# Kernel optimization log

Measured on AMD Instinct MI355X. Metric: run time of the kernel, lower is better.

Reference implementation:

```python
import jax, jax.numpy as jnp
import numpy as np

HEADS = 8

def _rotate_every_two(t):
    # t: [..., d]; interleaved rotation (-x2, x1) pairs
    x1 = t[..., ::2]
    x2 = t[..., 1::2]
    return jnp.stack([-x2, x1], axis=-1).reshape(t.shape)

def _theta_shift(t, sin, cos):
    return t * cos + _rotate_every_two(t) * sin

def setup_inputs() -> dict:
    key = jax.random.key(0)
    ks = jax.random.split(key, 5)
    B, H, W, C = 4, 40, 40, 512
    dh = C // HEADS
    x = jax.random.normal(ks[0], (B, H, W, C), dtype=jnp.float32)
    sin = jax.random.normal(ks[1], (H, W, dh), dtype=jnp.float32)
    cos = jax.random.normal(ks[2], (H, W, dh), dtype=jnp.float32)
    # 1x1 conv weight [3C, C] (kernel dims squeezed) + bias
    w_qkv = jax.random.normal(ks[3], (3 * C, C), dtype=jnp.float32) * (C ** -0.5)
    b_qkv = jnp.zeros((3 * C,), dtype=jnp.float32)
    return {"x": x, "sin": sin, "cos": cos, "w_qkv": w_qkv, "b_qkv": b_qkv}

def reference(x, sin, cos, w_qkv, b_qkv):
    B, H, W, C = x.shape
    heads = HEADS
    dh = C // heads
    scale = dh ** -0.5
    # 1x1 conv == per-pixel linear projection
    qkv = jnp.einsum('bhwc,oc->bhwo', x, w_qkv) + b_qkv  # [B,H,W,3C]
    q, k, v = jnp.split(qkv, 3, axis=-1)

    def to_heads(t):
        # channel order is (heads, dim_head) per the torch rearrange
        return t.reshape(B, H, W, heads, dh).transpose(0, 3, 1, 2, 4)  # [B,heads,H,W,dh]

    q = _theta_shift(to_heads(q), sin, cos)
    k = _theta_shift(to_heads(k), sin, cos)
    # v is computed but unused downstream in the original module (bug preserved)

    N = H * W
    q = q.reshape(B, heads, N, dh)
    k = k.reshape(B, heads, N, dh)

    attn = jnp.einsum('bhnd,bhmd->bhnm', q, k) * scale  # [B,heads,N,N]
    p = jax.nn.softmax(attn, axis=-1)
    # NOTE: original code does matmul(logist, kfine_heads) — K, not V. Kept faithful.
    out = jnp.einsum('bhnm,bhmd->bhnd', p, k)  # [B,heads,N,dh]
    out = out.transpose(0, 2, 1, 3).reshape(B, H, W, C)
    return out
```

## Files before the change

kernel.cpp:

```cpp
#include <hip/hip_runtime.h>
#include <hip/hip_bf16.h>


typedef __hip_bfloat16 bf16;
typedef __attribute__((ext_vector_type(8))) short short8;
typedef __attribute__((ext_vector_type(4))) short bfx4;
typedef __attribute__((ext_vector_type(4))) float f32x4;

#define NSP 1600
#define CDIM 512
#define DH 64

__device__ __forceinline__ f32x4 mfma32(short8 a, short8 b, f32x4 c) {
  return __builtin_amdgcn_mfma_f32_16x16x32_bf16(a, b, c, 0, 0, 0);
}

#if __has_builtin(__builtin_amdgcn_mfma_f32_16x16x16bf16_1k)
__device__ __forceinline__ f32x4 mfma_k16(bfx4 a, bfx4 b, f32x4 c) {
  return __builtin_amdgcn_mfma_f32_16x16x16bf16_1k(a, b, c, 0, 0, 0);
}
#else
__device__ __forceinline__ f32x4 mfma_k16(bfx4 a, bfx4 b, f32x4 c) {
  short8 a8 = {a.x, a.y, a.z, a.w, 0, 0, 0, 0};
  short8 b8 = {b.x, b.y, b.z, b.w, 0, 0, 0, 0};
  return __builtin_amdgcn_mfma_f32_16x16x32_bf16(a8, b8, c, 0, 0, 0);
}
#endif

__device__ __forceinline__ short8 cvt8(float4 v0, float4 v1) {
  short8 r; bf16* p = (bf16*)&r;
  p[0] = __float2bfloat16(v0.x); p[1] = __float2bfloat16(v0.y);
  p[2] = __float2bfloat16(v0.z); p[3] = __float2bfloat16(v0.w);
  p[4] = __float2bfloat16(v1.x); p[5] = __float2bfloat16(v1.y);
  p[6] = __float2bfloat16(v1.z); p[7] = __float2bfloat16(v1.w);
  return r;
}

extern "C" __global__ __launch_bounds__(256)
void cvt_kernel(const float* __restrict__ x, const float* __restrict__ w,
                const float* __restrict__ sin_t, const float* __restrict__ cos_t,
                bf16* __restrict__ x_bf, bf16* __restrict__ w_bf,
                float* __restrict__ sinT, float* __restrict__ cosT)
{
  __shared__ float t_lds[64][68];
  const int bid = blockIdx.x, tid = threadIdx.x;
  if (bid < 1600) {
    const size_t i = (size_t)bid * 2048 + tid * 8;
    float4 v0 = *(const float4*)(x + i);
    float4 v1 = *(const float4*)(x + i + 4);
    *(short8*)(x_bf + i) = cvt8(v0, v1);
  } else if (bid < 1856) {
    const size_t i = (size_t)(bid - 1600) * 2048 + tid * 8;
    float4 v0 = *(const float4*)(w + i);
    float4 v1 = *(const float4*)(w + i + 4);
    *(short8*)(w_bf + i) = cvt8(v0, v1);
  } else {
    const int t = bid - 1856;
    const float* src = (t < 25) ? sin_t : cos_t;
    float* dst = (t < 25) ? sinT : cosT;
    const int nt = (t < 25) ? t : t - 25;
    const int r = tid >> 2, c = (tid & 3) * 16;
#pragma unroll
    for (int j = 0; j < 4; ++j)
      *(float4*)&t_lds[r][c + j * 4] =
          *(const float4*)(src + (size_t)(nt * 64 + r) * 64 + c + j * 4);
    __syncthreads();
#pragma unroll
    for (int j4 = 0; j4 < 4; ++j4) {
      float4 o;
      o.x = t_lds[c + j4 * 4 + 0][r];
      o.y = t_lds[c + j4 * 4 + 1][r];
      o.z = t_lds[c + j4 * 4 + 2][r];
      o.w = t_lds[c + j4 * 4 + 3][r];
      *(float4*)(dst + (size_t)r * NSP + nt * 64 + c + j4 * 4) = o;
    }
  }
}

extern "C" __global__ __launch_bounds__(256)
void proj_kernel(const bf16* __restrict__ x_bf, const bf16* __restrict__ w_bf,
                 const float* __restrict__ bias, const float* __restrict__ sinT,
                 const float* __restrict__ cosT, bf16* __restrict__ q_ws,
                 bf16* __restrict__ k2_ws, bf16* __restrict__ kt2_ws)
{
  __shared__ __align__(16) char smem[36864];
  bf16 (*x_lds)[72] = (bf16(*)[72])smem;
  bf16 (*w_lds)[72] = (bf16(*)[72])(smem + 18432);
  bf16* ep = (bf16*)smem;

  const int tid  = threadIdx.x;
  const int wave = tid >> 6;
  const int lane = tid & 63;
  const int col  = lane & 15;
  const int quad = lane >> 4;
  const int wm = wave >> 1, wo = wave & 1;
  const int m0 = blockIdx.x * 128;
  const int o0 = blockIdx.y * 128;

  f32x4 acc[4][4];
#pragma unroll
  for (int i = 0; i < 4; ++i)
#pragma unroll
    for (int j = 0; j < 4; ++j) acc[i][j] = {0.f, 0.f, 0.f, 0.f};

  const int srow = tid >> 1;
  const int sch  = (tid & 1) * 32;

  for (int kt = 0; kt < 8; ++kt) {
    __syncthreads();
    {
      const bf16* xs = x_bf + (size_t)(m0 + srow) * CDIM + kt * 64 + sch;
      const bf16* ws = w_bf + (size_t)(o0 + srow) * CDIM + kt * 64 + sch;
#pragma unroll
      for (int j = 0; j < 4; ++j) {
        *(short8*)&x_lds[srow][sch + j * 8] = *(const short8*)(xs + j * 8);
        *(short8*)&w_lds[srow][sch + j * 8] = *(const short8*)(ws + j * 8);
      }
    }
    __syncthreads();
#pragma unroll
    for (int half = 0; half < 2; ++half) {
      short8 af[4], bfr[4];
#pragma unroll
      for (int mt = 0; mt < 4; ++mt)
        af[mt] = *(short8*)&x_lds[wm * 64 + mt * 16 + col][half * 32 + quad * 8];
#pragma unroll
      for (int ot = 0; ot < 4; ++ot)
        bfr[ot] = *(short8*)&w_lds[wo * 64 + ot * 16 + col][half * 32 + quad * 8];
#pragma unroll
      for (int mt = 0; mt < 4; ++mt)
#pragma unroll
        for (int ot = 0; ot < 4; ++ot)
          acc[mt][ot] = mfma32(af[mt], bfr[ot], acc[mt][ot]);
    }
  }

  __syncthreads();
  const int b_idx = (m0 + wm * 64) / NSP;
  const int n0w   = m0 + wm * 64 - b_idx * NSP;
  const bool isq  = (o0 < 512);
#pragma unroll
  for (int ot = 0; ot < 4; ++ot) {
    const int o_local = wo * 64 + ot * 16 + col;
    const int o_g = o0 + o_local;
    const float bv = bias[o_g];
    const int d = o_g & 63;
#pragma unroll
    for (int mt = 0; mt < 4; ++mt) {
      const int nl = mt * 16 + quad * 4;
      float t[4], rot[4];
#pragma unroll
      for (int r = 0; r < 4; ++r) t[r] = acc[mt][ot][r] + bv;
#pragma unroll
      for (int r = 0; r < 4; ++r) {
        float tp = __shfl_xor(t[r], 1, 64);
        rot[r] = (lane & 1) ? tp : -tp;
      }
      const float4 c4 = *(const float4*)(cosT + (size_t)d * NSP + n0w + nl);
      const float4 s4 = *(const float4*)(sinT + (size_t)d * NSP + n0w + nl);
      float res[4];
      res[0] = t[0] * c4.x + rot[0] * s4.x;
      res[1] = t[1] * c4.y + rot[1] * s4.y;
      res[2] = t[2] * c4.z + rot[2] * s4.z;
      res[3] = t[3] * c4.w + rot[3] * s4.w;
      if (isq) {
#pragma unroll
        for (int r = 0; r < 4; ++r) res[r] *= 0.125f;
      }
      bfx4 pk; bf16* pp = (bf16*)&pk;
#pragma unroll
      for (int r = 0; r < 4; ++r) pp[r] = __float2bfloat16(res[r]);
      *(bfx4*)&ep[o_local * 132 + wm * 64 + nl] = pk;
    }
  }
  __syncthreads();

  if (isq) {
    const int m_l = tid >> 1, half = tid & 1;
    const int gm = m0 + m_l;
    const int bi = gm / NSP, n = gm - bi * NSP;
    const int h = (o0 >> 6) + half;
    bf16* base = q_ws + ((size_t)(bi * 8 + h) * NSP + n) * 64;
#pragma unroll
    for (int c = 0; c < 8; ++c) {
      short8 v; bf16* vp = (bf16*)&v;
#pragma unroll
      for (int j = 0; j < 8; ++j) vp[j] = ep[(half * 64 + c * 8 + j) * 132 + m_l];
      *(short8*)(base + c * 8) = v;
    }
  } else {
    const int h0 = (o0 - 512) >> 6;
#pragma unroll
    for (int it = 0; it < 8; ++it) {
      const int ci = it * 256 + tid;
      const int hh = ci >> 10, T = (ci >> 9) & 1, inner = ci & 511;
      const int ccol = inner & 15, cq = (inner >> 4) & 3;
      const int f = (inner >> 6) & 1, ti = (inner >> 7) & 1, kh2 = (inner >> 8) & 1;
      const int gmb = m0 + T * 64;
      const int bi = gmb / NSP, ktile = (gmb - bi * NSP) >> 6;
      const int m_l = T * 64 + (2 * kh2 + ti) * 16 + ccol;
      const int er0 = hh * 64 + (f * 4 + cq) * 8;
      short8 v; bf16* vp = (bf16*)&v;
#pragma unroll
      for (int j = 0; j < 8; ++j) vp[j] = ep[(er0 + j) * 132 + m_l];
      *(short8*)(k2_ws +
          (((size_t)(bi * 8 + h0 + hh) * 25 + ktile) * 512 + inner) * 8) = v;
    }
#pragma unroll
    for (int it = 0; it < 8; ++it) {
      const int ci = it * 256 + tid;
      const int hh = ci >> 10, T = (ci >> 9) & 1, inner = ci & 511;
      const int ccol = inner & 15, cq = (inner >> 4) & 3;
      const int dt = (inner >> 6) & 3, kh2 = (inner >> 8) & 1;
      const int gmb = m0 + T * 64;
      const int bi = gmb / NSP, ktile = (gmb - bi * NSP) >> 6;
      const bf16* eprow =
          ep + (hh * 64 + dt * 16 + ccol) * 132 + T * 64 + kh2 * 32 + cq * 4;
      short8 v;
      ((bfx4*)&v)[0] = *(const bfx4*)(eprow);
      ((bfx4*)&v)[1] = *(const bfx4*)(eprow + 16);
      *(short8*)(kt2_ws +
          (((size_t)(bi * 8 + h0 + hh) * 25 + ktile) * 512 + inner) * 8) = v;
    }
  }
}

extern "C" __global__ __launch_bounds__(256)
void attn_kernel(const bf16* __restrict__ q_ws, const bf16* __restrict__ k2_ws,
                 const bf16* __restrict__ kt2_ws, float* __restrict__ out)
{
  __shared__ float red[2][64][36];

  const int qt = blockIdx.x, bh = blockIdx.y;
  const int b = bh >> 3, h = bh & 7;
  const int tid  = threadIdx.x;
  const int wave = tid >> 6;
  const int lane = tid & 63;
  const int col  = lane & 15;
  const int quad = lane >> 4;
  const int qg = wave & 1, kh = wave >> 1;

  short8 qb[2][2];
#pragma unroll
  for (int ct = 0; ct < 2; ++ct) {
    const bf16* qp =
        q_ws + ((size_t)bh * NSP + qt * 64 + (qg * 2 + ct) * 16 + col) * 64;
    qb[ct][0] = *(const short8*)(qp + quad * 8);
    qb[ct][1] = *(const short8*)(qp + 32 + quad * 8);
  }

  f32x4 oacc[4][2];
#pragma unroll
  for (int i = 0; i < 4; ++i)
#pragma unroll
    for (int j = 0; j < 2; ++j) oacc[i][j] = {0.f, 0.f, 0.f, 0.f};
  float l_part[2] = {0.f, 0.f};

  const bf16* k2b  = k2_ws  + (size_t)bh * 25 * 4096;
  const bf16* kt2b = kt2_ws + (size_t)bh * 25 * 4096;

  for (int kt = 0; kt < 25; ++kt) {
    const bf16* kc  = k2b  + kt * 4096;
    const bf16* kc2 = kt2b + kt * 4096;

    short8 kf[2][2];
#pragma unroll
    for (int ti = 0; ti < 2; ++ti)
#pragma unroll
      for (int f = 0; f < 2; ++f)
        kf[ti][f] =
            *(const short8*)(kc + (((kh * 2 + ti) * 2 + f) * 64 + lane) * 8);
    short8 ktf[4];
#pragma unroll
    for (int dt = 0; dt < 4; ++dt)
      ktf[dt] = *(const short8*)(kc2 + ((kh * 4 + dt) * 64 + lane) * 8);

    f32x4 s[2][2];
#pragma unroll
    for (int ti = 0; ti < 2; ++ti)
#pragma unroll
      for (int ct = 0; ct < 2; ++ct) {
        f32x4 t = {0.f, 0.f, 0.f, 0.f};
        t = mfma32(kf[ti][0], qb[ct][0], t);
        t = mfma32(kf[ti][1], qb[ct][1], t);
        s[ti][ct] = t;
      }

    bfx4 p4[2][2];
#pragma unroll
    for (int ti = 0; ti < 2; ++ti)
#pragma unroll
      for (int ct = 0; ct < 2; ++ct) {
#pragma unroll
        for (int r = 0; r < 4; ++r) s[ti][ct][r] = __expf(s[ti][ct][r]);
        l_part[ct] += s[ti][ct][0] + s[ti][ct][1] + s[ti][ct][2] + s[ti][ct][3];
        bf16* pp = (bf16*)&p4[ti][ct];
#pragma unroll
        for (int r = 0; r < 4; ++r) pp[r] = __float2bfloat16(s[ti][ct][r]);
      }

#pragma unroll
    for (int dt = 0; dt < 4; ++dt) {
      bfx4 alo = __builtin_shufflevector(ktf[dt], ktf[dt], 0, 1, 2, 3);
      bfx4 ahi = __builtin_shufflevector(ktf[dt], ktf[dt], 4, 5, 6, 7);
#pragma unroll
      for (int ct = 0; ct < 2; ++ct) {
        oacc[dt][ct] = mfma_k16(alo, p4[0][ct], oacc[dt][ct]);
        oacc[dt][ct] = mfma_k16(ahi, p4[1][ct], oacc[dt][ct]);
      }
    }
  }

#pragma unroll
  for (int ct = 0; ct < 2; ++ct) {
    l_part[ct] += __shfl_xor(l_part[ct], 16, 64);
    l_part[ct] += __shfl_xor(l_part[ct], 32, 64);
  }

  if (wave >= 2) {
    float* dst = &red[wave - 2][lane][0];
#pragma unroll
    for (int dt = 0; dt < 4; ++dt)
#pragma unroll
      for (int ct = 0; ct < 2; ++ct)
        *(f32x4*)(dst + (dt * 2 + ct) * 4) = oacc[dt][ct];
    dst[32] = l_part[0]; dst[33] = l_part[1];
  }
  __syncthreads();
  if (wave < 2) {
    const float* srcr = &red[wave][lane][0];
#pragma unroll
    for (int dt = 0; dt < 4; ++dt)
#pragma unroll
      for (int ct = 0; ct < 2; ++ct)
        oacc[dt][ct] += *(const f32x4*)(srcr + (dt * 2 + ct) * 4);
    const float inv0 = 1.f / (l_part[0] + srcr[32]);
    const float inv1 = 1.f / (l_part[1] + srcr[33]);
#pragma unroll
    for (int ct = 0; ct < 2; ++ct) {
      const float inv = ct ? inv1 : inv0;
      const int qrow = qt * 64 + (qg * 2 + ct) * 16 + col;
      float* ob = out + ((size_t)b * NSP + qrow) * CDIM + h * 64;
#pragma unroll
      for (int dt = 0; dt < 4; ++dt) {
        float4 v;
        v.x = oacc[dt][ct][0] * inv; v.y = oacc[dt][ct][1] * inv;
        v.z = oacc[dt][ct][2] * inv; v.w = oacc[dt][ct][3] * inv;
        *(float4*)(ob + dt * 16 + quad * 4) = v;
      }
    }
  }
}

extern "C" void kernel_launch(void* const* d_in, const int* in_sizes, int n_in,
                              void* d_out, int out_size, void* d_ws, size_t ws_size,
                              hipStream_t stream) {
  const float* x     = (const float*)d_in[0];
  const float* sin_t = (const float*)d_in[1];
  const float* cos_t = (const float*)d_in[2];
  const float* w_qkv = (const float*)d_in[3];
  const float* b_qkv = (const float*)d_in[4];
  float* out = (float*)d_out;

  const size_t QK = (size_t)32 * NSP * DH;
  bf16* q_ws   = (bf16*)d_ws;
  bf16* k2_ws  = q_ws + QK;
  bf16* kt2_ws = k2_ws + QK;
  bf16* x_bf   = kt2_ws + QK;
  bf16* w_bf   = x_bf + (size_t)6400 * CDIM;
  float* sinT  = (float*)(w_bf + (size_t)1024 * CDIM);
  float* cosT  = sinT + (size_t)DH * NSP;

  cvt_kernel<<<1906, 256, 0, stream>>>(x, w_qkv, sin_t, cos_t, x_bf, w_bf, sinT, cosT);

  dim3 gproj(50, 8);
  proj_kernel<<<gproj, 256, 0, stream>>>(x_bf, w_bf, b_qkv, sinT, cosT,
                                         q_ws, k2_ws, kt2_ws);

  dim3 gattn(25, 32);
  attn_kernel<<<gattn, 256, 0, stream>>>(q_ws, k2_ws, kt2_ws, out);
}
```

Before: 139.5 us.

## Split attention key tiles across eight waves with two-stage cross-wave reduction

The attention kernel now launches 512 threads (8 waves) per block instead of 4. Each wave handles one 16-key sub-tile instead of two, so the per-wave MFMA chain per key tile is halved. Partial outputs and row sums are combined in LDS through a two-stage tree reduction. The aim is more waves in flight to hide latency on a grid of only 800 blocks, at the cost of an extra barrier, more LDS, and redundant Q loads per wave.

```diff
diff --git a/kernel.cpp b/kernel.cpp
--- a/kernel.cpp
+++ b/kernel.cpp
@@ -225,11 +225,11 @@
   }
 }
 
-extern "C" __global__ __launch_bounds__(256)
+extern "C" __global__ __launch_bounds__(512, 6)
 void attn_kernel(const bf16* __restrict__ q_ws, const bf16* __restrict__ k2_ws,
                  const bf16* __restrict__ kt2_ws, float* __restrict__ out)
 {
-  __shared__ float red[2][64][36];
+  __shared__ float red[4][64][36];
 
   const int qt = blockIdx.x, bh = blockIdx.y;
   const int b = bh >> 3, h = bh & 7;
@@ -238,7 +238,8 @@
   const int lane = tid & 63;
   const int col  = lane & 15;
   const int quad = lane >> 4;
-  const int qg = wave & 1, kh = wave >> 1;
+  const int qg = wave & 1;
+  const int kh = wave >> 1;
 
   short8 qb[2][2];
 #pragma unroll
@@ -258,57 +259,46 @@
 
   const bf16* k2b  = k2_ws  + (size_t)bh * 25 * 4096;
   const bf16* kt2b = kt2_ws + (size_t)bh * 25 * 4096;
+  const int khh = kh >> 1, khl = kh & 1;
 
   for (int kt = 0; kt < 25; ++kt) {
     const bf16* kc  = k2b  + kt * 4096;
     const bf16* kc2 = kt2b + kt * 4096;
 
-    short8 kf[2][2];
-#pragma unroll
-    for (int ti = 0; ti < 2; ++ti)
-#pragma unroll
-      for (int f = 0; f < 2; ++f)
-        kf[ti][f] =
-            *(const short8*)(kc + (((kh * 2 + ti) * 2 + f) * 64 + lane) * 8);
-    short8 ktf[4];
-#pragma unroll
-    for (int dt = 0; dt < 4; ++dt)
-      ktf[dt] = *(const short8*)(kc2 + ((kh * 4 + dt) * 64 + lane) * 8);
-
-    f32x4 s[2][2];
-#pragma unroll
-    for (int ti = 0; ti < 2; ++ti)
-#pragma unroll
-      for (int ct = 0; ct < 2; ++ct) {
-        f32x4 t = {0.f, 0.f, 0.f, 0.f};
-        t = mfma32(kf[ti][0], qb[ct][0], t);
-        t = mfma32(kf[ti][1], qb[ct][1], t);
-        s[ti][ct] = t;
-      }
-
-    bfx4 p4[2][2];
-#pragma unroll
-    for (int ti = 0; ti < 2; ++ti)
-#pragma unroll
-      for (int ct = 0; ct < 2; ++ct) {
-#pragma unroll
-        for (int r = 0; r < 4; ++r) s[ti][ct][r] = __expf(s[ti][ct][r]);
-        l_part[ct] += s[ti][ct][0] + s[ti][ct][1] + s[ti][ct][2] + s[ti][ct][3];
-        bf16* pp = (bf16*)&p4[ti][ct];
-#pragma unroll
-        for (int r = 0; r < 4; ++r) pp[r] = __float2bfloat16(s[ti][ct][r]);
-      }
-
-#pragma unroll
-    for (int dt = 0; dt < 4; ++dt) {
-      bfx4 alo = __builtin_shufflevector(ktf[dt], ktf[dt], 0, 1, 2, 3);
-      bfx4 ahi = __builtin_shufflevector(ktf[dt], ktf[dt], 4, 5, 6, 7);
-#pragma unroll
-      for (int ct = 0; ct < 2; ++ct) {
-        oacc[dt][ct] = mfma_k16(alo, p4[0][ct], oacc[dt][ct]);
-        oacc[dt][ct] = mfma_k16(ahi, p4[1][ct], oacc[dt][ct]);
-      }
-    }
+    short8 kf[2];
+#pragma unroll
+    for (int f = 0; f < 2; ++f)
+      kf[f] = *(const short8*)(kc + (((kh * 2 + f) * 64) + lane) * 8);
+    bfx4 ktf[4];
+#pragma unroll
+    for (int dt = 0; dt < 4; ++dt)
+      ktf[dt] = *(const bfx4*)(kc2 + (((khh * 4 + dt) * 64 + lane) * 8) + khl * 4);
+
+    f32x4 s[2];
+#pragma unroll
+    for (int ct = 0; ct < 2; ++ct) {
+      f32x4 t = {0.f, 0.f, 0.f, 0.f};
+      t = mfma32(kf[0], qb[ct][0], t);
+      t = mfma32(kf[1], qb[ct][1], t);
+      s[ct] = t;
+    }
+
+    bfx4 p4[2];
+#pragma unroll
+    for (int ct = 0; ct < 2; ++ct) {
+#pragma unroll
+      for (int r = 0; r < 4; ++r) s[ct][r] = __expf(s[ct][r]);
+      l_part[ct] += s[ct][0] + s[ct][1] + s[ct][2] + s[ct][3];
+      bf16* pp = (bf16*)&p4[ct];
+#pragma unroll
+      for (int r = 0; r < 4; ++r) pp[r] = __float2bfloat16(s[ct][r]);
+    }
+
+#pragma unroll
+    for (int dt = 0; dt < 4; ++dt)
+#pragma unroll
+      for (int ct = 0; ct < 2; ++ct)
+        oacc[dt][ct] = mfma_k16(ktf[dt], p4[ct], oacc[dt][ct]);
   }
 
 #pragma unroll
@@ -317,7 +307,27 @@
     l_part[ct] += __shfl_xor(l_part[ct], 32, 64);
   }
 
-  if (wave >= 2) {
+  if (wave >= 4) {
+    float* dst = &red[wave - 4][lane][0];
+#pragma unroll
+    for (int dt = 0; dt < 4; ++dt)
+#pragma unroll
+      for (int ct = 0; ct < 2; ++ct)
+        *(f32x4*)(dst + (dt * 2 + ct) * 4) = oacc[dt][ct];
+    dst[32] = l_part[0]; dst[33] = l_part[1];
+  }
+  __syncthreads();
+  if (wave < 4) {
+    const float* srcr = &red[wave][lane][0];
+#pragma unroll
+    for (int dt = 0; dt < 4; ++dt)
+#pragma unroll
+      for (int ct = 0; ct < 2; ++ct)
+        oacc[dt][ct] += *(const f32x4*)(srcr + (dt * 2 + ct) * 4);
+    l_part[0] += srcr[32]; l_part[1] += srcr[33];
+  }
+  __syncthreads();
+  if (wave == 2 || wave == 3) {
     float* dst = &red[wave - 2][lane][0];
 #pragma unroll
     for (int dt = 0; dt < 4; ++dt)
@@ -378,5 +388,5 @@
                                          q_ws, k2_ws, kt2_ws);
 
   dim3 gattn(25, 32);
-  attn_kernel<<<gattn, 256, 0, stream>>>(q_ws, k2_ws, kt2_ws, out);
-}
+  attn_kernel<<<gattn, 512, 0, stream>>>(q_ws, k2_ws, kt2_ws, out);
+}
```

New measurement: 149.6 us. 1.07x slower.

## Double-buffer K fragment loads and remap attention grid for XCD locality

Applied to the files above, without the earlier changes.

The attention loop now prefetches the next key tile's register fragments while computing on the current one, using two register buffers in a manually unrolled ping-pong loop. This is meant to hide global load latency behind the MFMA and exp work. The grid becomes a 1D launch of 800 blocks, with block index mapped so that consecutive IDs modulo 8 land on different batch-heads. This likely aims to keep all blocks of a given batch-head on the same XCD so they share its L2. The cost is higher register pressure from the doubled fragments, which could lower occupancy.

```diff
diff --git a/kernel.cpp b/kernel.cpp
--- a/kernel.cpp
+++ b/kernel.cpp
@@ -225,13 +225,69 @@
   }
 }
 
+
+#define LOADF(KF, KTF, KT)                                                    \
+  {                                                                           \
+    const bf16* kc_  = k2b  + (KT) * 4096;                                    \
+    const bf16* kc2_ = kt2b + (KT) * 4096;                                    \
+    _Pragma("unroll")                                                         \
+    for (int ti = 0; ti < 2; ++ti)                                            \
+      _Pragma("unroll")                                                       \
+      for (int f = 0; f < 2; ++f)                                             \
+        KF[ti][f] =                                                           \
+            *(const short8*)(kc_ + (((kh * 2 + ti) * 2 + f) * 64 + lane) * 8);\
+    _Pragma("unroll")                                                         \
+    for (int dt = 0; dt < 4; ++dt)                                            \
+      KTF[dt] = *(const short8*)(kc2_ + ((kh * 4 + dt) * 64 + lane) * 8);     \
+  }
+
+#define COMPUTEF(KF, KTF)                                                     \
+  {                                                                           \
+    f32x4 s[2][2];                                                            \
+    _Pragma("unroll")                                                         \
+    for (int ti = 0; ti < 2; ++ti)                                            \
+      _Pragma("unroll")                                                       \
+      for (int ct = 0; ct < 2; ++ct) {                                        \
+        f32x4 t = {0.f, 0.f, 0.f, 0.f};                                       \
+        t = mfma32(KF[ti][0], qb[ct][0], t);                                  \
+        t = mfma32(KF[ti][1], qb[ct][1], t);                                  \
+        s[ti][ct] = t;                                                        \
+      }                                                                       \
+    bfx4 p4[2][2];                                                            \
+    _Pragma("unroll")                                                         \
+    for (int ti = 0; ti < 2; ++ti)                                            \
+      _Pragma("unroll")                                                       \
+      for (int ct = 0; ct < 2; ++ct) {                                        \
+        _Pragma("unroll")                                                     \
+        for (int r = 0; r < 4; ++r) s[ti][ct][r] = __expf(s[ti][ct][r]);      \
+        l_part[ct] +=                                                         \
+            s[ti][ct][0] + s[ti][ct][1] + s[ti][ct][2] + s[ti][ct][3];        \
+        bf16* pp = (bf16*)&p4[ti][ct];                                        \
+        _Pragma("unroll")                                                     \
+        for (int r = 0; r < 4; ++r) pp[r] = __float2bfloat16(s[ti][ct][r]);   \
+      }                                                                       \
+    _Pragma("unroll")                                                         \
+    for (int dt = 0; dt < 4; ++dt) {                                          \
+      bfx4 alo = __builtin_shufflevector(KTF[dt], KTF[dt], 0, 1, 2, 3);       \
+      bfx4 ahi = __builtin_shufflevector(KTF[dt], KTF[dt], 4, 5, 6, 7);       \
+      _Pragma("unroll")                                                       \
+      for (int ct = 0; ct < 2; ++ct) {                                        \
+        oacc[dt][ct] = mfma_k16(alo, p4[0][ct], oacc[dt][ct]);                \
+        oacc[dt][ct] = mfma_k16(ahi, p4[1][ct], oacc[dt][ct]);                \
+      }                                                                       \
+    }                                                                         \
+  }
+
 extern "C" __global__ __launch_bounds__(256)
 void attn_kernel(const bf16* __restrict__ q_ws, const bf16* __restrict__ k2_ws,
                  const bf16* __restrict__ kt2_ws, float* __restrict__ out)
 {
   __shared__ float red[2][64][36];
 
-  const int qt = blockIdx.x, bh = blockIdx.y;
+  const int id = blockIdx.x;
+  const int xr = id & 7, inner = id >> 3;
+  const int qt = inner % 25;
+  const int bh = (inner / 25) * 8 + xr;
   const int b = bh >> 3, h = bh & 7;
   const int tid  = threadIdx.x;
   const int wave = tid >> 6;
@@ -259,57 +315,16 @@
   const bf16* k2b  = k2_ws  + (size_t)bh * 25 * 4096;
   const bf16* kt2b = kt2_ws + (size_t)bh * 25 * 4096;
 
-  for (int kt = 0; kt < 25; ++kt) {
-    const bf16* kc  = k2b  + kt * 4096;
-    const bf16* kc2 = kt2b + kt * 4096;
-
-    short8 kf[2][2];
-#pragma unroll
-    for (int ti = 0; ti < 2; ++ti)
-#pragma unroll
-      for (int f = 0; f < 2; ++f)
-        kf[ti][f] =
-            *(const short8*)(kc + (((kh * 2 + ti) * 2 + f) * 64 + lane) * 8);
-    short8 ktf[4];
-#pragma unroll
-    for (int dt = 0; dt < 4; ++dt)
-      ktf[dt] = *(const short8*)(kc2 + ((kh * 4 + dt) * 64 + lane) * 8);
-
-    f32x4 s[2][2];
-#pragma unroll
-    for (int ti = 0; ti < 2; ++ti)
-#pragma unroll
-      for (int ct = 0; ct < 2; ++ct) {
-        f32x4 t = {0.f, 0.f, 0.f, 0.f};
-        t = mfma32(kf[ti][0], qb[ct][0], t);
-        t = mfma32(kf[ti][1], qb[ct][1], t);
-        s[ti][ct] = t;
-      }
-
-    bfx4 p4[2][2];
-#pragma unroll
-    for (int ti = 0; ti < 2; ++ti)
-#pragma unroll
-      for (int ct = 0; ct < 2; ++ct) {
-#pragma unroll
-        for (int r = 0; r < 4; ++r) s[ti][ct][r] = __expf(s[ti][ct][r]);
-        l_part[ct] += s[ti][ct][0] + s[ti][ct][1] + s[ti][ct][2] + s[ti][ct][3];
-        bf16* pp = (bf16*)&p4[ti][ct];
-#pragma unroll
-        for (int r = 0; r < 4; ++r) pp[r] = __float2bfloat16(s[ti][ct][r]);
-      }
-
-#pragma unroll
-    for (int dt = 0; dt < 4; ++dt) {
-      bfx4 alo = __builtin_shufflevector(ktf[dt], ktf[dt], 0, 1, 2, 3);
-      bfx4 ahi = __builtin_shufflevector(ktf[dt], ktf[dt], 4, 5, 6, 7);
-#pragma unroll
-      for (int ct = 0; ct < 2; ++ct) {
-        oacc[dt][ct] = mfma_k16(alo, p4[0][ct], oacc[dt][ct]);
-        oacc[dt][ct] = mfma_k16(ahi, p4[1][ct], oacc[dt][ct]);
-      }
-    }
-  }
+  short8 kfA[2][2], ktfA[4], kfB[2][2], ktfB[4];
+  LOADF(kfA, ktfA, 0)
+#pragma unroll 1
+  for (int i = 0; i < 12; ++i) {
+    LOADF(kfB, ktfB, 2 * i + 1)
+    COMPUTEF(kfA, ktfA)
+    LOADF(kfA, ktfA, 2 * i + 2)
+    COMPUTEF(kfB, ktfB)
+  }
+  COMPUTEF(kfA, ktfA)
 
 #pragma unroll
   for (int ct = 0; ct < 2; ++ct) {
@@ -377,6 +392,5 @@
   proj_kernel<<<gproj, 256, 0, stream>>>(x_bf, w_bf, b_qkv, sinT, cosT,
                                          q_ws, k2_ws, kt2_ws);
 
-  dim3 gattn(25, 32);
-  attn_kernel<<<gattn, 256, 0, stream>>>(q_ws, k2_ws, kt2_ws, out);
-}
+  attn_kernel<<<800, 256, 0, stream>>>(q_ws, k2_ws, kt2_ws, out);
+}
```

Result: no change. 137.5 us (-1.5%).
